# Performance work log

Measured on AMD Instinct MI355X. Metric: run time of the kernel, lower is better.

## Reference

```python
import jax, jax.numpy as jnp
import numpy as np

N, D, SPC = 4096, 128, 8  # batch, embed dim, samples per class
MARGIN = 0.2


def setup_inputs() -> dict:
    key = jax.random.key(0)
    k1, k2 = jax.random.split(key)
    embeddings = jax.random.normal(k1, (N, D), dtype=jnp.float32)
    embeddings1 = jax.random.normal(k2, (N, D), dtype=jnp.float32)
    # Balanced labels: 512 classes x 8 samples -> every row has SPC-1 positives,
    # which is required for the original module's pairing logic to be well-defined.
    labels = (jnp.arange(N) // SPC).astype(jnp.int32)
    return {
        "embeddings": embeddings,
        "product_labels": labels,
        "embeddings1": embeddings1,
        "prod_labels1": labels,
        "k_ret": SPC - 1,  # = int(sum(positives)) // N for balanced labels
    }


def reference(embeddings, product_labels, embeddings1, prod_labels1, k_ret):
    n = embeddings.shape[0]
    # --- get_distance: d2[i,j] = mm[i,i] + mm[j,j] - 2*mm[i,j], clamped then sqrt ---
    mm = embeddings @ embeddings1.T                      # [N, N]
    diag = jnp.diagonal(mm)[:, None]                     # [N, 1]
    d2 = jnp.maximum(diag + diag.T - 2.0 * mm, 0.0)
    distance = jnp.sqrt(jnp.maximum(d2, 1e-4))           # clamp(min=0).clamp(min=1e-4).sqrt()
    # --- positive / negative masks (eq - eye; nonzero picks values != 0) ---
    eq = (prod_labels1[:, None] == product_labels[None, :]).astype(jnp.float32)
    pos_vals = eq - jnp.eye(n, dtype=jnp.float32)
    pos_nz = pos_vals != 0.0                             # torch .nonzero() semantics (incl. -1)
    n_ids = (pos_vals > 0.0).astype(jnp.float32)
    neg_scores = n_ids * 1e6 + distance                  # push positives out of bottom-k
    # --- bottom-k negatives per row (topk largest=False), then scatter+nonzero == sorted idx ---
    _, neg_idx = jax.lax.top_k(-neg_scores, k_ret)       # k smallest distances among negatives
    neg_sorted = jnp.sort(neg_idx, axis=1)               # ascending, as .nonzero() would return
    # --- positive indices per row in ascending order (stable argsort of mask) ---
    pos_sorted = jnp.argsort(jnp.logical_not(pos_nz), axis=1, stable=True)[:, :k_ret]
    has_pos = jnp.take_along_axis(pos_nz, pos_sorted, axis=1)  # all True for balanced batch
    # --- pairwise filter: d(a,p) < d(a,n) + margin ---
    d_pos_sel = jnp.take_along_axis(distance, pos_sorted, axis=1)
    d_neg_sel = jnp.take_along_axis(distance, neg_sorted, axis=1)
    valid = (d_pos_sel < d_neg_sel + MARGIN) & has_pos   # [N, k]
    # --- triplet loss on selected (anchor, pos, neg) from `embeddings` ---
    a = embeddings[:, None, :]                           # [N, 1, D]
    p = embeddings[pos_sorted]                           # [N, k, D]
    g = embeddings[neg_sorted]                           # [N, k, D]
    d_ap = jnp.sqrt(jnp.sum((p - a) ** 2, axis=-1) + 1e-8)
    d_an = jnp.sqrt(jnp.sum((g - a) ** 2, axis=-1) + 1e-8)
    pos_loss = jax.nn.relu(d_ap + MARGIN)
    neg_loss = jax.nn.relu(MARGIN - d_an)
    vm = valid.astype(jnp.float32)
    loss_sum = jnp.sum(vm * (pos_loss + neg_loss))
    active = ((pos_loss > 0.0) | (neg_loss > 0.0)).astype(jnp.float32)
    count = jnp.sum(vm * active)
    return jnp.where(count > 0.0, loss_sum / count, loss_sum)
```

## Files before the change

### kernel.cpp

```cpp
#include <hip/hip_runtime.h>
#include <math.h>

#define NROWS 4096
#define D 128
#define SPC 8
#define KRET 7
#define MARGIN 0.2f
#define NTILE 32
#define CPR (NTILE * KRET)

typedef unsigned long long u64;
typedef unsigned int u32;
typedef __attribute__((ext_vector_type(8))) short short8;
typedef __attribute__((ext_vector_type(16))) float f32x16;

__device__ __forceinline__ u32 minu32(u32 a, u32 b) { return a < b ? a : b; }
__device__ __forceinline__ u32 maxu32(u32 a, u32 b) { return a > b ? a : b; }

__device__ __forceinline__ ushort f2bf_rne(float x) {
    unsigned u = __float_as_uint(x);
    unsigned r = (u + 0x7fffu + ((u >> 16) & 1u)) >> 16;
    return (ushort)r;
}

__device__ __forceinline__ void ins7(u32 (&s)[KRET], u32 pk) {
#pragma unroll
    for (int k = 0; k < KRET; ++k) {
        const u32 lo = minu32(s[k], pk);
        pk = maxu32(s[k], pk);
        s[k] = lo;
    }
}

__device__ __forceinline__ void ins7x2(u32 (&s)[KRET], u32 q0, u32 q1) {
    s[6] = minu32(s[6], minu32(maxu32(s[5], q0), maxu32(s[4], q1)));
    s[5] = minu32(s[5], minu32(maxu32(s[4], q0), maxu32(s[3], q1)));
    s[4] = minu32(s[4], minu32(maxu32(s[3], q0), maxu32(s[2], q1)));
    s[3] = minu32(s[3], minu32(maxu32(s[2], q0), maxu32(s[1], q1)));
    s[2] = minu32(s[2], minu32(maxu32(s[1], q0), maxu32(s[0], q1)));
    s[1] = minu32(s[1], minu32(maxu32(s[0], q0), q1));
    s[0] = minu32(s[0], q0);
}


__global__ __launch_bounds__(256) void prep_kernel(const float* __restrict__ emb,
                                                   const float* __restrict__ emb1,
                                                   ushort* __restrict__ embH,
                                                   ushort* __restrict__ emb1H,
                                                   float* __restrict__ diag) {
    const int lane = threadIdx.x & 63;
    const int row = blockIdx.x * 4 + (threadIdx.x >> 6);
    const size_t base = (size_t)row * D + 2 * lane;
    const float2 a = *(const float2*)(emb + base);
    const float2 b = *(const float2*)(emb1 + base);

    *(ushort2*)(embH + base)  = make_ushort2(f2bf_rne(a.x), f2bf_rne(a.y));
    *(ushort2*)(emb1H + base) = make_ushort2(f2bf_rne(b.x), f2bf_rne(b.y));

    float s = a.x * b.x + a.y * b.y;
#pragma unroll
    for (int off = 1; off < 64; off <<= 1) s += __shfl_xor(s, off, 64);
    if (lane == 0) diag[row] = s;
}

__global__ __launch_bounds__(256, 4) void dist_mfma(const ushort* __restrict__ embH,
                                                    const ushort* __restrict__ emb1H,
                                                    const int* __restrict__ labels,
                                                    const int* __restrict__ labels1,
                                                    const float* __restrict__ diag,
                                                    float* __restrict__ posd, u32* __restrict__ cand) {
    __shared__ ushort smem[2][9216];
    __shared__ float sdA[128], sdB[128];
    __shared__ int sLi[128], sLj[128];
    __shared__ int s_lmin[4], s_lmax[4];
    ushort* AH = smem[0];
    ushort* BH = smem[1];

    const int t = threadIdx.x;
    const int i0 = blockIdx.y * 128, j0 = blockIdx.x * 128;
    const int w = t >> 6, l = t & 63;

    {
        int lab;
        if (t < 128) { sdA[t] = diag[i0 + t]; lab = labels1[i0 + t]; sLi[t] = lab; }
        else         { sdB[t - 128] = diag[j0 + t - 128]; lab = labels[j0 + t - 128]; sLj[t - 128] = lab; }
        int mn = lab, mx = lab;
#pragma unroll
        for (int off = 1; off < 64; off <<= 1) {
            mn = min(mn, __shfl_xor(mn, off, 64));
            mx = max(mx, __shfl_xor(mx, off, 64));
        }
        if (l == 0) { s_lmin[w] = mn; s_lmax[w] = mx; }
    }

    const int il = l & 31;
    const int hi = l >> 5;
    const int irow = w * 32 + il;

    f32x16 acc[4];
#pragma unroll
    for (int n = 0; n < 4; ++n)
#pragma unroll
        for (int r = 0; r < 16; ++r) acc[n][r] = 0.f;

    bool hasPos = false;
    const int srow = t & 127;
    for (int p = 0; p < 2; ++p) {
        if (p) __syncthreads();
#pragma unroll
        for (int n = 0; n < 4; ++n) {
            const int c = n * 2 + (t >> 7);
            const size_t gA = (size_t)(i0 + srow) * D + p * 64 + c * 8;
            const size_t gB = (size_t)(j0 + srow) * D + p * 64 + c * 8;
            const int ld = srow * 72 + c * 8;
            *(uint4*)(AH + ld) = *(const uint4*)(embH + gA);
            *(uint4*)(BH + ld) = *(const uint4*)(emb1H + gB);
        }
        __syncthreads();

        if (p == 0) {
            const int minLi = min(s_lmin[0], s_lmin[1]);
            const int maxLi = max(s_lmax[0], s_lmax[1]);
            const int minLj = min(s_lmin[2], s_lmin[3]);
            const int maxLj = max(s_lmax[2], s_lmax[3]);
            hasPos = !(maxLi < minLj || maxLj < minLi);
        }

#pragma unroll
        for (int kk = 0; kk < 4; ++kk) {
            const int ko = kk * 16 + hi * 8;
            const short8 bfr = *(const short8*)(AH + irow * 72 + ko);
#pragma unroll
            for (int n = 0; n < 4; ++n) {
                const short8 afr = *(const short8*)(BH + (n * 32 + il) * 72 + ko);
                acc[n] = __builtin_amdgcn_mfma_f32_32x32x16_bf16(afr, bfr, acc[n], 0, 0, 0);
            }
        }
    }

    const float di = sdA[irow];
    const int gi = i0 + irow;
    const int li = hasPos ? sLi[irow] : 0;

    u32 s[KRET];
#pragma unroll
    for (int k = 0; k < KRET; ++k) s[k] = 0xFFFFFFFFu;

#pragma unroll
    for (int n = 0; n < 4; ++n) {
#pragma unroll
        for (int g = 0; g < 4; ++g) {
            const int jb = n * 32 + 8 * g + 4 * hi;
            const float4 dj4 = *(const float4*)(sdB + jb);
            const float djv[4] = {dj4.x, dj4.y, dj4.z, dj4.w};
            u32 pk[4];
            if (!hasPos) {
#pragma unroll
                for (int q = 0; q < 4; ++q) {
                    const int r = g * 4 + q;
                    const float d2c = fmaxf(fmaf(-2.f, acc[n][r], di + djv[q]), 1e-4f);
                    pk[q] = (__float_as_uint(d2c) & 0xFFFF0000u) | (u32)(j0 + jb + q);
                }
            } else {
                const int4 lj4 = *(const int4*)(sLj + jb);
                const int ljv[4] = {lj4.x, lj4.y, lj4.z, lj4.w};
#pragma unroll
                for (int q = 0; q < 4; ++q) {
                    const int r = g * 4 + q;
                    const int gj = j0 + jb + q;
                    const float d2c = fmaxf(fmaf(-2.f, acc[n][r], di + djv[q]), 1e-4f);
                    const bool pos = (ljv[q] == li) && (gi != gj);
                    if (pos) posd[(size_t)gi * SPC + (gj & (SPC - 1))] = d2c;
                    pk[q] = (pos ? 0xFFFF0000u : (__float_as_uint(d2c) & 0xFFFF0000u)) | (u32)gj;
                }
            }
            {
                const u32 q0 = minu32(pk[0], pk[1]), q1 = maxu32(pk[0], pk[1]);
                if (q0 < s[KRET - 1]) ins7x2(s, q0, q1);
            }
            {
                const u32 q0 = minu32(pk[2], pk[3]), q1 = maxu32(pk[2], pk[3]);
                if (q0 < s[KRET - 1]) ins7x2(s, q0, q1);
            }
        }
    }

    u32 o[KRET];
#pragma unroll
    for (int k = 0; k < KRET; ++k) o[k] = (u32)__shfl_xor((int)s[k], 32, 64);
#pragma unroll
    for (int k = 0; k < KRET; ++k) if (o[k] < s[KRET - 1]) ins7(s, o[k]);

    if (hi == 0) {
        u32* cw = cand + (size_t)gi * CPR + (j0 >> 7) * KRET;
#pragma unroll
        for (int k = 0; k < KRET; ++k) cw[k] = s[k];
    }
}

__global__ __launch_bounds__(256) void merge_kernel(const float* __restrict__ emb,
                                                    const float* __restrict__ posd,
                                                    const u32* __restrict__ cand,
                                                    float* __restrict__ rowls,
                                                    float* __restrict__ rowcnt) {
    const int lane = threadIdx.x & 63;
    const int i = blockIdx.x * 4 + (threadIdx.x >> 6);
    const u32* cr = cand + (size_t)i * CPR;
    u32 e[4];
    e[0] = cr[lane];
    e[1] = cr[64 + lane];
    e[2] = cr[128 + lane];
    e[3] = (lane < CPR - 192) ? cr[192 + lane] : 0xFFFFFFFFu;

    u32 w[KRET];
#pragma unroll
    for (int r = 0; r < KRET; ++r) {
        u32 m = minu32(minu32(e[0], e[1]), minu32(e[2], e[3]));
#pragma unroll
        for (int off = 1; off < 64; off <<= 1) m = minu32(m, (u32)__shfl_xor((int)m, off, 64));
        w[r] = m;
#pragma unroll
        for (int q = 0; q < 4; ++q) e[q] = (e[q] == m) ? 0xFFFFFFFFu : e[q];
    }

    u32 s[8];
#pragma unroll
    for (int r = 0; r < KRET; ++r) s[r] = (w[r] << 20) | (w[r] >> 12);
    s[7] = 0xFFFFFFFFu;
#define CE(x, y) { u32 lo = minu32(s[x], s[y]); u32 hi2 = maxu32(s[x], s[y]); s[x] = lo; s[y] = hi2; }
    CE(0,1) CE(2,3) CE(4,5) CE(6,7)
    CE(0,2) CE(1,3) CE(4,6) CE(5,7)
    CE(1,2) CE(5,6)
    CE(0,4) CE(1,5) CE(2,6) CE(3,7)
    CE(2,4) CE(3,5)
    CE(1,2) CE(3,4) CE(5,6)
#undef CE

    const int ig = i & (SPC - 1);
    float ls = 0.f, cnt = 0.f;
    bool any = false;
    bool v[KRET];
    int nidx[KRET];
#pragma unroll
    for (int k = 0; k < KRET; ++k) {
        nidx[k] = (int)(s[k] >> 20);
        const float d2n = __uint_as_float(((s[k] >> 4) & 0xFFFF0u) << 12);
        const float dneg = sqrtf(d2n);
        const int m = k + (k >= ig ? 1 : 0);
        const float dp = sqrtf(posd[(size_t)i * SPC + m]);
        v[k] = dp < dneg + MARGIN;
        any = any || v[k];
    }

    if (any) {
        const float a0 = emb[(size_t)i * D + lane];
        const float a1 = emb[(size_t)i * D + 64 + lane];
#pragma unroll
        for (int k = 0; k < KRET; ++k) {
            if (v[k]) {
                const int m = k + (k >= ig ? 1 : 0);
                const int tp = (i & ~(SPC - 1)) + m;
                const int tn = nidx[k];
                float d0 = emb[(size_t)tp * D + lane] - a0;
                float d1 = emb[(size_t)tp * D + 64 + lane] - a1;
                float sp = d0 * d0 + d1 * d1;
                float g0 = emb[(size_t)tn * D + lane] - a0;
                float g1 = emb[(size_t)tn * D + 64 + lane] - a1;
                float sn = g0 * g0 + g1 * g1;
#pragma unroll
                for (int off = 1; off < 64; off <<= 1) {
                    sp += __shfl_xor(sp, off, 64);
                    sn += __shfl_xor(sn, off, 64);
                }
                ls += (sqrtf(sp + 1e-8f) + MARGIN) + fmaxf(MARGIN - sqrtf(sn + 1e-8f), 0.f);
                cnt += 1.f;
            }
        }
    }
    if (lane == 0) {
        rowls[i] = ls;
        rowcnt[i] = cnt;
    }
}

__global__ __launch_bounds__(256) void finalize_kernel(const float* __restrict__ rowls,
                                                       const float* __restrict__ rowcnt,
                                                       float* __restrict__ out) {
    const int t = threadIdx.x;
    __shared__ float sls[4], scnt[4];
    float ls = 0.f, cnt = 0.f;
#pragma unroll
    for (int q = 0; q < NROWS / 256; ++q) {
        ls += rowls[q * 256 + t];
        cnt += rowcnt[q * 256 + t];
    }
#pragma unroll
    for (int off = 1; off < 64; off <<= 1) {
        ls += __shfl_xor(ls, off, 64);
        cnt += __shfl_xor(cnt, off, 64);
    }
    if ((t & 63) == 0) { sls[t >> 6] = ls; scnt[t >> 6] = cnt; }
    __syncthreads();
    if (t == 0) {
        float L = sls[0] + sls[1] + sls[2] + sls[3];
        float C = scnt[0] + scnt[1] + scnt[2] + scnt[3];
        out[0] = C > 0.f ? L / C : L;
    }
}

__global__ __launch_bounds__(256) void diag_kernel(const float* __restrict__ emb,
                                                   const float* __restrict__ emb1,
                                                   float* __restrict__ diag) {
    int wave = threadIdx.x >> 6;
    int lane = threadIdx.x & 63;
    int row = blockIdx.x * 4 + wave;
    const float* a = emb + (size_t)row * D;
    const float* b = emb1 + (size_t)row * D;
    float s = a[lane] * b[lane] + a[lane + 64] * b[lane + 64];
    for (int off = 32; off > 0; off >>= 1) s += __shfl_down(s, off, 64);
    if (lane == 0) diag[row] = s;
}

__global__ __launch_bounds__(256) void main_kernel(const float* __restrict__ emb,
                                                   const float* __restrict__ emb1,
                                                   const int* __restrict__ labels,
                                                   const int* __restrict__ labels1,
                                                   const float* __restrict__ diag,
                                                   float* __restrict__ ws_acc) {
    const int i = blockIdx.x;
    const int tid = threadIdx.x;
    __shared__ float s_anchor[D];
    __shared__ float s_posd[SPC];
    __shared__ u64 s_red[4];
    __shared__ u64 s_win;
    __shared__ int s_negidx[KRET];
    __shared__ float s_negd[KRET];
    __shared__ float s_dreal[2 * KRET];

    if (tid < D) s_anchor[tid] = emb[(size_t)i * D + tid];
    __syncthreads();
    const float diag_i = diag[i];
    const int li = labels1[i];
    float score[16];
#pragma unroll
    for (int it = 0; it < 16; ++it) {
        int j = it * 256 + tid;
        const float4* r = (const float4*)(emb1 + (size_t)j * D);
        float acc = 0.f;
#pragma unroll
        for (int q = 0; q < D / 4; ++q) {
            float4 vv = r[q];
            acc = fmaf(vv.x, s_anchor[4 * q + 0], acc);
            acc = fmaf(vv.y, s_anchor[4 * q + 1], acc);
            acc = fmaf(vv.z, s_anchor[4 * q + 2], acc);
            acc = fmaf(vv.w, s_anchor[4 * q + 3], acc);
        }
        float d2 = diag_i + diag[j] - 2.f * acc;
        float dist = sqrtf(fmaxf(d2, 1e-4f));
        bool is_pos = (labels[j] == li) && (j != i);
        if (is_pos) s_posd[j & (SPC - 1)] = dist;
        score[it] = dist + (is_pos ? 1e6f : 0.f);
    }
    __syncthreads();
    for (int r = 0; r < KRET; ++r) {
        u64 best = ~0ull;
#pragma unroll
        for (int it = 0; it < 16; ++it) {
            u64 p = ((u64)__float_as_uint(score[it]) << 32) | (unsigned)(it * 256 + tid);
            best = best < p ? best : p;
        }
        for (int off = 32; off > 0; off >>= 1) {
            u64 o = __shfl_down(best, off, 64);
            best = best < o ? best : o;
        }
        if ((tid & 63) == 0) s_red[tid >> 6] = best;
        __syncthreads();
        if (tid == 0) {
            u64 w2 = s_red[0];
            w2 = w2 < s_red[1] ? w2 : s_red[1];
            w2 = w2 < s_red[2] ? w2 : s_red[2];
            w2 = w2 < s_red[3] ? w2 : s_red[3];
            s_win = w2;
        }
        __syncthreads();
        u64 w2 = s_win;
        int cj = (int)(w2 & 0xffffffffu);
        if (tid == (cj & 255)) score[cj >> 8] = 1e30f;
        if (tid == 0) { s_negidx[r] = cj; s_negd[r] = __uint_as_float((unsigned)(w2 >> 32)); }
        __syncthreads();
    }
    if (tid == 0) {
        for (int a = 1; a < KRET; ++a) {
            int ix = s_negidx[a]; float dv = s_negd[a];
            int b = a - 1;
            while (b >= 0 && s_negidx[b] > ix) {
                s_negidx[b + 1] = s_negidx[b]; s_negd[b + 1] = s_negd[b]; --b;
            }
            s_negidx[b + 1] = ix; s_negd[b + 1] = dv;
        }
    }
    __syncthreads();
    {
        int wave = tid >> 6, lane = tid & 63;
        int gb = i & ~(SPC - 1);
        for (int p = wave; p < 2 * KRET; p += 4) {
            int tgt;
            if (p < KRET) {
                int k = p;
                int m = k + (k >= (i & (SPC - 1)) ? 1 : 0);
                tgt = gb + m;
            } else tgt = s_negidx[p - KRET];
            float d0 = emb[(size_t)tgt * D + lane] - s_anchor[lane];
            float d1 = emb[(size_t)tgt * D + 64 + lane] - s_anchor[64 + lane];
            float s = d0 * d0 + d1 * d1;
            for (int off = 32; off > 0; off >>= 1) s += __shfl_down(s, off, 64);
            if (lane == 0) s_dreal[p] = sqrtf(s + 1e-8f);
        }
    }
    __syncthreads();
    if (tid == 0) {
        float ls = 0.f, cnt = 0.f;
        for (int k = 0; k < KRET; ++k) {
            int m = k + (k >= (i & (SPC - 1)) ? 1 : 0);
            if (s_posd[m] < s_negd[k] + MARGIN) {
                ls += (s_dreal[k] + MARGIN) + fmaxf(MARGIN - s_dreal[KRET + k], 0.f);
                cnt += 1.f;
            }
        }
        if (ls != 0.f) atomicAdd(&ws_acc[0], ls);
        if (cnt != 0.f) atomicAdd(&ws_acc[1], cnt);
    }
}

__global__ void finalize_ws(const float* __restrict__ ws_acc, float* __restrict__ out) {
    float ls = ws_acc[0], cnt = ws_acc[1];
    out[0] = cnt > 0.f ? ls / cnt : ls;
}

extern "C" void kernel_launch(void* const* d_in, const int* in_sizes, int n_in,
                              void* d_out, int out_size, void* d_ws, size_t ws_size,
                              hipStream_t stream) {
    const float* emb     = (const float*)d_in[0];
    const int*   labels  = (const int*)d_in[1];
    const float* emb1    = (const float*)d_in[2];
    const int*   labels1 = (const int*)d_in[3];
    float* ws = (float*)d_ws;

    const size_t need = (size_t)2015232 * sizeof(float);
    if (ws_size >= need) {
        float*  diag   = ws + 4096;
        float*  posd   = ws + 8192;
        ushort* embH   = (ushort*)(ws + 40960);
        ushort* emb1H  = (ushort*)(ws + 106496);
        u32*    cand   = (u32*)(ws + 172032);
        float*  rowls  = ws + 2007040;
        float*  rowcnt = ws + 2011136;

        prep_kernel<<<NROWS / 4, 256, 0, stream>>>(emb, emb1, embH, emb1H, diag);
        dim3 grid(NROWS / 128, NROWS / 128);
        dist_mfma<<<grid, 256, 0, stream>>>(embH, emb1H, labels, labels1, diag, posd, cand);
        merge_kernel<<<NROWS / 4, 256, 0, stream>>>(emb, posd, cand, rowls, rowcnt);
        finalize_kernel<<<1, 256, 0, stream>>>(rowls, rowcnt, (float*)d_out);
    } else {
        hipMemsetAsync(d_ws, 0, 2 * sizeof(float), stream);
        float* diag = ws + 2;
        diag_kernel<<<NROWS / 4, 256, 0, stream>>>(emb, emb1, diag);
        main_kernel<<<NROWS, 256, 0, stream>>>(emb, emb1, labels, labels1, diag, ws);
        finalize_ws<<<1, 1, 0, stream>>>(ws, (float*)d_out);
    }
}
```

Before: 39.24 us.

## Pre-swizzle bf16 embeddings into MFMA fragment layout and drop LDS staging

```diff
diff --git a/kernel.cpp b/kernel.cpp
--- a/kernel.cpp
+++ b/kernel.cpp
@@ -19,8 +19,10 @@
 
 __device__ __forceinline__ ushort f2bf_rne(float x) {
     unsigned u = __float_as_uint(x);
-    unsigned r = (u + 0x7fffu + ((u >> 16) & 1u)) >> 16;
-    return (ushort)r;
+    return (ushort)((u + 0x7fffu + ((u >> 16) & 1u)) >> 16);
+}
+__device__ __forceinline__ u32 pack2bf(float lo, float hi) {
+    return (u32)f2bf_rne(lo) | ((u32)f2bf_rne(hi) << 16);
 }
 
 __device__ __forceinline__ void ins7(u32 (&s)[KRET], u32 pk) {
@@ -43,38 +45,49 @@
 }
 
 
-__global__ __launch_bounds__(256) void prep_kernel(const float* __restrict__ emb,
-                                                   const float* __restrict__ emb1,
-                                                   ushort* __restrict__ embH,
-                                                   ushort* __restrict__ emb1H,
-                                                   float* __restrict__ diag) {
-    const int lane = threadIdx.x & 63;
-    const int row = blockIdx.x * 4 + (threadIdx.x >> 6);
-    const size_t base = (size_t)row * D + 2 * lane;
-    const float2 a = *(const float2*)(emb + base);
-    const float2 b = *(const float2*)(emb1 + base);
-
-    *(ushort2*)(embH + base)  = make_ushort2(f2bf_rne(a.x), f2bf_rne(a.y));
-    *(ushort2*)(emb1H + base) = make_ushort2(f2bf_rne(b.x), f2bf_rne(b.y));
-
-    float s = a.x * b.x + a.y * b.y;
-#pragma unroll
-    for (int off = 1; off < 64; off <<= 1) s += __shfl_xor(s, off, 64);
-    if (lane == 0) diag[row] = s;
-}
-
-__global__ __launch_bounds__(256, 4) void dist_mfma(const ushort* __restrict__ embH,
-                                                    const ushort* __restrict__ emb1H,
+__global__ __launch_bounds__(64) void prep_kernel(const float* __restrict__ emb,
+                                                  const float* __restrict__ emb1,
+                                                  ushort* __restrict__ embF,
+                                                  ushort* __restrict__ emb1F,
+                                                  float* __restrict__ diag) {
+    const int l = threadIdx.x;
+    const int g = blockIdx.x;
+    const int il = l & 31, hi = l >> 5;
+    const int row = g * 32 + il;
+    const float* pa = emb  + (size_t)row * D;
+    const float* pb = emb1 + (size_t)row * D;
+    float dacc = 0.f;
+#pragma unroll
+    for (int kkg = 0; kkg < 8; ++kkg) {
+        const int k0 = kkg * 16 + hi * 8;
+        const float4 a0 = *(const float4*)(pa + k0);
+        const float4 a1 = *(const float4*)(pa + k0 + 4);
+        const float4 b0 = *(const float4*)(pb + k0);
+        const float4 b1 = *(const float4*)(pb + k0 + 4);
+        dacc += a0.x * b0.x + a0.y * b0.y + a0.z * b0.z + a0.w * b0.w;
+        dacc += a1.x * b1.x + a1.y * b1.y + a1.z * b1.z + a1.w * b1.w;
+        uint4 ua, ub;
+        ua.x = pack2bf(a0.x, a0.y); ua.y = pack2bf(a0.z, a0.w);
+        ua.z = pack2bf(a1.x, a1.y); ua.w = pack2bf(a1.z, a1.w);
+        ub.x = pack2bf(b0.x, b0.y); ub.y = pack2bf(b0.z, b0.w);
+        ub.z = pack2bf(b1.x, b1.y); ub.w = pack2bf(b1.z, b1.w);
+        const size_t dst = ((size_t)(g * 8 + kkg) * 2 + hi) * 256 + il * 8;
+        *(uint4*)(embF + dst)  = ua;
+        *(uint4*)(emb1F + dst) = ub;
+    }
+    dacc += __shfl_xor(dacc, 32, 64);
+    if (hi == 0) diag[row] = dacc;
+}
+
+__global__ __launch_bounds__(256, 4) void dist_mfma(const ushort* __restrict__ embF,
+                                                    const ushort* __restrict__ emb1F,
                                                     const int* __restrict__ labels,
                                                     const int* __restrict__ labels1,
                                                     const float* __restrict__ diag,
                                                     float* __restrict__ posd, u32* __restrict__ cand) {
-    __shared__ ushort smem[2][9216];
     __shared__ float sdA[128], sdB[128];
     __shared__ int sLi[128], sLj[128];
     __shared__ int s_lmin[4], s_lmax[4];
-    ushort* AH = smem[0];
-    ushort* BH = smem[1];
 
     const int t = threadIdx.x;
     const int i0 = blockIdx.y * 128, j0 = blockIdx.x * 128;
@@ -92,10 +105,17 @@
         }
         if (l == 0) { s_lmin[w] = mn; s_lmax[w] = mx; }
     }
+    __syncthreads();
+
+    const bool hasPos = !((max(s_lmax[0], s_lmax[1]) < min(s_lmin[2], s_lmin[3])) ||
+                          (max(s_lmax[2], s_lmax[3]) < min(s_lmin[0], s_lmin[1])));
 
     const int il = l & 31;
     const int hi = l >> 5;
     const int irow = w * 32 + il;
+    const int laneoff = hi * 256 + il * 8;
+    const ushort* Ab = embF  + ((size_t)(blockIdx.y * 4 + w) * 8) * 512 + laneoff;
+    const ushort* Bb = emb1F + ((size_t)(blockIdx.x * 4) * 8) * 512 + laneoff;
 
     f32x16 acc[4];
 #pragma unroll
@@ -103,38 +123,13 @@
 #pragma unroll
         for (int r = 0; r < 16; ++r) acc[n][r] = 0.f;
 
-    bool hasPos = false;
-    const int srow = t & 127;
-    for (int p = 0; p < 2; ++p) {
-        if (p) __syncthreads();
+#pragma unroll
+    for (int kkg = 0; kkg < 8; ++kkg) {
+        const short8 bfr = *(const short8*)(Ab + (size_t)kkg * 512);
 #pragma unroll
         for (int n = 0; n < 4; ++n) {
-            const int c = n * 2 + (t >> 7);
-            const size_t gA = (size_t)(i0 + srow) * D + p * 64 + c * 8;
-            const size_t gB = (size_t)(j0 + srow) * D + p * 64 + c * 8;
-            const int ld = srow * 72 + c * 8;
-            *(uint4*)(AH + ld) = *(const uint4*)(embH + gA);
-            *(uint4*)(BH + ld) = *(const uint4*)(emb1H + gB);
-        }
-        __syncthreads();
-
-        if (p == 0) {
-            const int minLi = min(s_lmin[0], s_lmin[1]);
-            const int maxLi = max(s_lmax[0], s_lmax[1]);
-            const int minLj = min(s_lmin[2], s_lmin[3]);
-            const int maxLj = max(s_lmax[2], s_lmax[3]);
-            hasPos = !(maxLi < minLj || maxLj < minLi);
-        }
-
-#pragma unroll
-        for (int kk = 0; kk < 4; ++kk) {
-            const int ko = kk * 16 + hi * 8;
-            const short8 bfr = *(const short8*)(AH + irow * 72 + ko);
-#pragma unroll
-            for (int n = 0; n < 4; ++n) {
-                const short8 afr = *(const short8*)(BH + (n * 32 + il) * 72 + ko);
-                acc[n] = __builtin_amdgcn_mfma_f32_32x32x16_bf16(afr, bfr, acc[n], 0, 0, 0);
-            }
+            const short8 afr = *(const short8*)(Bb + (size_t)(n * 8 + kkg) * 512);
+            acc[n] = __builtin_amdgcn_mfma_f32_32x32x16_bf16(afr, bfr, acc[n], 0, 0, 0);
         }
     }
 
@@ -446,19 +441,19 @@
     const int*   labels1 = (const int*)d_in[3];
     float* ws = (float*)d_ws;
 
-    const size_t need = (size_t)2015232 * sizeof(float);
+    const size_t need = (size_t)1515520 * sizeof(float);
     if (ws_size >= need) {
         float*  diag   = ws + 4096;
         float*  posd   = ws + 8192;
-        ushort* embH   = (ushort*)(ws + 40960);
-        ushort* emb1H  = (ushort*)(ws + 106496);
-        u32*    cand   = (u32*)(ws + 172032);
-        float*  rowls  = ws + 2007040;
-        float*  rowcnt = ws + 2011136;
-
-        prep_kernel<<<NROWS / 4, 256, 0, stream>>>(emb, emb1, embH, emb1H, diag);
+        ushort* embF   = (ushort*)(ws + 65536);
+        ushort* emb1F  = (ushort*)(ws + 327680);
+        u32*    cand   = (u32*)(ws + 589824);
+        float*  rowls  = ws + 1507328;
+        float*  rowcnt = ws + 1511424;
+
+        prep_kernel<<<NROWS / 32, 64, 0, stream>>>(emb, emb1, embF, emb1F, diag);
         dim3 grid(NROWS / 128, NROWS / 128);
-        dist_mfma<<<grid, 256, 0, stream>>>(embH, emb1H, labels, labels1, diag, posd, cand);
+        dist_mfma<<<grid, 256, 0, stream>>>(embF, emb1F, labels, labels1, diag, posd, cand);
         merge_kernel<<<NROWS / 4, 256, 0, stream>>>(emb, posd, cand, rowls, rowcnt);
         finalize_kernel<<<1, 256, 0, stream>>>(rowls, rowcnt, (float*)d_out);
     } else {
```

Result: no change. 39.64 us (+1.0%).
